# Kernel tuning notes

Measured on AMD Instinct MI355X. Metric: run time of the kernel, lower is better.

## Reference

```python
import jax, jax.numpy as jnp
import numpy as np

N, E, F_IN, H, D = 50000, 800000, 128, 4, 32
NEG_SLOPE = 0.2

def setup_inputs() -> dict:
    key = jax.random.key(0)
    ks = jax.random.split(key, 8)
    x = jax.random.normal(ks[0], (N, F_IN), dtype=jnp.float32)
    src = jax.random.randint(ks[1], (E,), 0, N, dtype=jnp.int32)
    dst = jax.random.randint(ks[2], (E,), 0, N, dtype=jnp.int32)
    s = 1.0 / np.sqrt(F_IN)
    W_src = jax.random.uniform(ks[3], (F_IN, H * D), jnp.float32, -s, s)
    b_src = jnp.zeros((H * D,), jnp.float32)
    W_dst = jax.random.uniform(ks[4], (F_IN, H * D), jnp.float32, -s, s)
    b_dst = jnp.zeros((H * D,), jnp.float32)
    attn = jax.random.normal(ks[5], (H, D), dtype=jnp.float32) / np.sqrt(D)
    return {"x": x, "src": src, "dst": dst, "W_src": W_src, "b_src": b_src,
            "W_dst": W_dst, "b_dst": b_dst, "attn": attn}

def reference(x, src, dst, W_src, b_src, W_dst, b_dst, attn):
    n = x.shape[0]
    # dense projections: [N, H, D]
    fs = (x @ W_src + b_src).reshape(n, H, D)
    fd = (x @ W_dst + b_dst).reshape(n, H, D)
    # GATv2 edge score: a^T leaky_relu(W_l x_u + W_r x_v)
    e = jax.nn.leaky_relu(fs[src] + fd[dst], NEG_SLOPE)  # [E, H, D]
    score = jnp.einsum('ehd,hd->eh', e, attn)            # [E, H]
    # segment softmax over incoming edges of each dst node
    smax = jax.ops.segment_max(score, dst, num_segments=n)
    smax = jnp.where(jnp.isfinite(smax), smax, 0.0)
    ex = jnp.exp(score - smax[dst])
    denom = jax.ops.segment_sum(ex, dst, num_segments=n)
    alpha = ex / denom[dst]                              # [E, H]
    # scatter-weighted aggregation of src features
    h = jax.ops.segment_sum(alpha[:, :, None] * fs[src], dst, num_segments=n)
    h = jax.nn.relu(h)                                   # activation=relu
    return h.reshape(n, H * D)
```

## Files before the change

kernel.cpp:

```cpp
#include <hip/hip_runtime.h>
#include <hip/hip_fp16.h>

#define NN 50000
#define NE 800000
#define FIN 128
#define NH 4
#define HD 32
#define FOUT 128
#define NEG 0.2f
#define NB_W    ((256 * FIN + 255) / 256)
#define N_GEMM  391
#define NBKT    98
#define CHUNK   4096
#define NCHUNK  ((NE + CHUNK - 1) / CHUNK)
#define GB_GRID (NCHUNK * 3)
#define BCAP    12288

typedef __attribute__((ext_vector_type(8))) short bf16x8;
typedef __attribute__((ext_vector_type(4))) float f32x4;

__device__ __forceinline__ uint f2bf_u(float f) {
    uint u = __float_as_uint(f);
    u += 0x7FFF + ((u >> 16) & 1);
    return u >> 16;
}
__device__ __forceinline__ ushort f2bf(float f) { return (ushort)f2bf_u(f); }

template<int CTRL>
__device__ __forceinline__ float dpp_add(float x) {
    int y = __builtin_amdgcn_update_dpp(0, __float_as_int(x), CTRL, 0xF, 0xF, false);
    return x + __int_as_float(y);
}
#define DPP_QUAD_XOR1 0xB1
#define DPP_QUAD_XOR2 0x4E

__device__ __forceinline__ __half2 u2h(uint u) { return __builtin_bit_cast(__half2, u); }
__device__ __forceinline__ uint h2u(__half2 h) { return __builtin_bit_cast(uint, h); }

__device__ __forceinline__ __half2 hmax2(__half2 a, __half2 b) {
    uint r, ua = h2u(a), ub = h2u(b);
    asm("v_pk_max_f16 %0, %1, %2" : "=v"(r) : "v"(ua), "v"(ub));
    return u2h(r);
}

__global__ __launch_bounds__(256) void hist_wt_k(
    const int* __restrict__ dst, int* __restrict__ chunk_hist,
    const float* __restrict__ Wsrc, const float* __restrict__ Wdst,
    ushort* __restrict__ Wt)
{
    __shared__ int hist[NBKT];
    const int b = blockIdx.x;
    const int tid = threadIdx.x;
    if (b < NCHUNK) {
        const int e0 = b * CHUNK;
        for (int t = tid; t < NBKT; t += 256) hist[t] = 0;
        __syncthreads();
        #pragma unroll
        for (int k = 0; k < 16; ++k) {
            const int e = e0 + k * 256 + tid;
            if (e < NE) atomicAdd(&hist[dst[e] >> 9], 1);
        }
        __syncthreads();
        for (int t = tid; t < NBKT; t += 256)
            chunk_hist[b * NBKT + t] = hist[t];
    } else {
        int t = (b - NCHUNK) * 256 + tid;
        if (t >= 256 * FIN) return;
        int n = t >> 7, k = t & 127;
        float v = (n < 128) ? Wsrc[k * 128 + n] : Wdst[k * 128 + (n - 128)];
        Wt[t] = f2bf(v);
    }
}

__global__ __launch_bounds__(256) void scan_chunks_k(
    const int* __restrict__ chunk_hist, int* __restrict__ chunk_base, int* __restrict__ btotal)
{
    __shared__ int sh[256];
    const int b = blockIdx.x, t = threadIdx.x;
    const int v = (t < NCHUNK) ? chunk_hist[t * NBKT + b] : 0;
    sh[t] = v;
    __syncthreads();
    for (int off = 1; off < 256; off <<= 1) {
        int add = (t >= off) ? sh[t - off] : 0;
        __syncthreads();
        sh[t] += add;
        __syncthreads();
    }
    if (t < NCHUNK) chunk_base[t * NBKT + b] = sh[t] - v;
    if (t == 255) btotal[b] = sh[255];
}

__global__ __launch_bounds__(256) void scan_buckets_k(
    const int* __restrict__ btotal, int* __restrict__ bkbase,
    const float* __restrict__ attn, __half* __restrict__ attn_h)
{
    __shared__ int sh[256];
    const int t = threadIdx.x;
    const int v = (t < NBKT) ? btotal[t] : 0;
    sh[t] = v;
    __syncthreads();
    for (int off = 1; off < 256; off <<= 1) {
        int add = (t >= off) ? sh[t - off] : 0;
        __syncthreads();
        sh[t] += add;
        __syncthreads();
    }
    if (t < NBKT) bkbase[t] = sh[t] - v;
    if (t == 0) bkbase[NBKT] = NE;
    if (t < FOUT) attn_h[t] = __float2half(attn[t]);
}

__global__ __launch_bounds__(256) void gemm_scatter_k(
    const float* __restrict__ x, const ushort* __restrict__ Wt,
    const float* __restrict__ bsrc, const float* __restrict__ bdst,
    __half* __restrict__ fsfd,
    const int* __restrict__ dst, const int* __restrict__ src,
    const int* __restrict__ bkbase, const int* __restrict__ chunk_base,
    uint* __restrict__ ebuf)
{
    __shared__ ushort As[128 * 128];
    __shared__ ushort Bs[64 * 128];
    __shared__ int cur[NBKT];
    const int b = blockIdx.x;
    const int tid = threadIdx.x;

    if (b % 3 == 0) {
        const int chunk = b / 3;
        for (int t = tid; t < NBKT; t += 256)
            cur[t] = bkbase[t] + chunk_base[chunk * NBKT + t];
        __syncthreads();
        const int e0 = chunk * CHUNK;
        #pragma unroll
        for (int k = 0; k < 16; ++k) {
            const int e = e0 + k * 256 + tid;
            if (e < NE) {
                const int d = dst[e];
                const int p = atomicAdd(&cur[d >> 9], 1);
                ebuf[p] = ((uint)d << 16) | (uint)src[e];
            }
        }
        return;
    }

    const int g = b - b / 3 - 1;
    if (g >= N_GEMM) return;
    const int bm = g * 128;

    for (int q = tid; q < 128 * 16; q += 256) {
        int r = q >> 4, c16 = q & 15;
        int row = bm + r;
        uint4 o = make_uint4(0u, 0u, 0u, 0u);
        if (row < NN) {
            const float4 a = *(const float4*)&x[(size_t)row * FIN + c16 * 8];
            const float4 c = *(const float4*)&x[(size_t)row * FIN + c16 * 8 + 4];
            o.x = f2bf_u(a.x) | (f2bf_u(a.y) << 16);
            o.y = f2bf_u(a.z) | (f2bf_u(a.w) << 16);
            o.z = f2bf_u(c.x) | (f2bf_u(c.y) << 16);
            o.w = f2bf_u(c.z) | (f2bf_u(c.w) << 16);
        }
        int off = r * 256 + ((c16 * 16) ^ ((r & 7) << 4));
        *(uint4*)((char*)As + off) = o;
    }

    const int wid = tid >> 6, lane = tid & 63;
    const int wr = (wid >> 1) * 64, wc = (wid & 1) * 32;
    const int lrow = lane & 15;
    const int lk = (lane >> 4) * 16;

    #pragma unroll
    for (int ct = 0; ct < 4; ++ct) {
        if (ct > 0) __syncthreads();
        for (int q = tid; q < 64 * 16; q += 256) {
            int r = q >> 4, c16 = q & 15;
            uint4 v = *(const uint4*)&Wt[(ct * 64 + r) * FIN + c16 * 8];
            int off = r * 256 + ((c16 * 16) ^ ((r & 7) << 4));
            *(uint4*)((char*)Bs + off) = v;
        }
        __syncthreads();

        f32x4 acc[4][2] = {};
        #pragma unroll
        for (int kk = 0; kk < 4; ++kk) {
            bf16x8 a[4], bb[2];
            #pragma unroll
            for (int m = 0; m < 4; ++m) {
                int r = wr + m * 16 + lrow;
                int off = r * 256 + ((kk * 64 + lk) ^ ((r & 7) << 4));
                a[m] = *(bf16x8*)((char*)As + off);
            }
            #pragma unroll
            for (int n = 0; n < 2; ++n) {
                int r = wc + n * 16 + lrow;
                int off = r * 256 + ((kk * 64 + lk) ^ ((r & 7) << 4));
                bb[n] = *(bf16x8*)((char*)Bs + off);
            }
            #pragma unroll
            for (int m = 0; m < 4; ++m)
                #pragma unroll
                for (int n = 0; n < 2; ++n)
                    acc[m][n] = __builtin_amdgcn_mfma_f32_16x16x32_bf16(a[m], bb[n], acc[m][n], 0, 0, 0);
        }

        #pragma unroll
        for (int m = 0; m < 4; ++m) {
            #pragma unroll
            for (int n = 0; n < 2; ++n) {
                int gcol = ct * 64 + wc + n * 16 + (lane & 15);
                float bias = (gcol < 128) ? bsrc[gcol] : bdst[gcol - 128];
                #pragma unroll
                for (int r = 0; r < 4; ++r) {
                    int grow = bm + wr + m * 16 + (lane >> 4) * 4 + r;
                    if (grow < NN)
                        fsfd[(size_t)grow * 256 + gcol] = __float2half(acc[m][n][r] + bias);
                }
            }
        }
    }
}

__global__ __launch_bounds__(256) void binB_k(
    const uint* __restrict__ ebuf, const int* __restrict__ bkbase,
    int* __restrict__ rowptr, ushort* __restrict__ nbr)
{
    __shared__ int cnt_s[512];
    __shared__ int ps[256];
    __shared__ ushort buf[BCAP];
    const int b = blockIdx.x;
    const int tid = threadIdx.x;
    const int node0 = b << 9;
    const int nodes = (node0 + 512 < NN) ? 512 : (NN - node0);
    const int segbase = bkbase[b];
    const int segend  = bkbase[b + 1];
    const int seglen  = segend - segbase;

    cnt_s[tid] = 0;
    cnt_s[tid + 256] = 0;
    __syncthreads();
    for (int i = segbase + tid; i < segend; i += 256)
        atomicAdd(&cnt_s[(int)(ebuf[i] >> 16) - node0], 1);
    __syncthreads();

    const int c0 = cnt_s[2 * tid], c1 = cnt_s[2 * tid + 1];
    const int pair = c0 + c1;
    ps[tid] = pair;
    __syncthreads();
    for (int off = 1; off < 256; off <<= 1) {
        int add = (tid >= off) ? ps[tid - off] : 0;
        __syncthreads();
        ps[tid] += add;
        __syncthreads();
    }
    const int ex = ps[tid] - pair;
    __syncthreads();
    cnt_s[2 * tid] = ex;
    cnt_s[2 * tid + 1] = ex + c0;
    if (2 * tid < nodes)     rowptr[node0 + 2 * tid]     = segbase + ex;
    if (2 * tid + 1 < nodes) rowptr[node0 + 2 * tid + 1] = segbase + ex + c0;
    if (b == NBKT - 1 && tid == 0) rowptr[NN] = segend;
    __syncthreads();

    if (seglen <= BCAP) {
        for (int i = segbase + tid; i < segend; i += 256) {
            const uint e = ebuf[i];
            const int d = (int)(e >> 16) - node0;
            const int p = atomicAdd(&cnt_s[d], 1);
            buf[p] = (ushort)(e & 0xffffu);
        }
        __syncthreads();
        for (int i = tid; i < seglen; i += 256)
            nbr[segbase + i] = buf[i];
    } else {
        for (int i = segbase + tid; i < segend; i += 256) {
            const uint e = ebuf[i];
            const int d = (int)(e >> 16) - node0;
            const int p = atomicAdd(&cnt_s[d], 1);
            nbr[segbase + p] = (ushort)(e & 0xffffu);
        }
    }
}

__global__ __launch_bounds__(256) void gat_node_k(
    const __half* __restrict__ fsfd, const __half* __restrict__ attn_h,
    const int* __restrict__ rowptr, const ushort* __restrict__ nbr,
    float* __restrict__ out)
{
    const int node = blockIdx.x * 4 + (threadIdx.x >> 6);
    const int lane = threadIdx.x & 63;
    const int ql = lane & 15;
    const int q  = lane >> 4;

    const uint4 ufd = *(const uint4*)&fsfd[(size_t)node * 256 + 128 + 8 * ql];
    const __half2 fd0 = u2h(ufd.x), fd1 = u2h(ufd.y), fd2 = u2h(ufd.z), fd3 = u2h(ufd.w);
    const uint4 uav = *(const uint4*)&attn_h[8 * ql];
    const __half2 av0 = u2h(uav.x), av1 = u2h(uav.y), av2 = u2h(uav.z), av3 = u2h(uav.w);
    const __half2 k02 = __float2half2_rn(NEG);

    const int beg = rowptr[node];
    const int end = rowptr[node + 1];

    float den = 0.f;
    __half2 acc0 = u2h(0), acc1 = u2h(0), acc2 = u2h(0), acc3 = u2h(0);

    for (int i = beg; i < end; i += 16) {
        #pragma unroll
        for (int j = 0; j < 4; ++j) {
            const int idx = i + 4 * j + q;
            const bool valid = idx < end;
            const int s = nbr[valid ? idx : end - 1];
            const uint4 u = *(const uint4*)&fsfd[(size_t)s * 256 + 8 * ql];
            const __half2 f0 = u2h(u.x), f1 = u2h(u.y), f2 = u2h(u.z), f3 = u2h(u.w);
            __half2 v0 = __hadd2(f0, fd0), v1 = __hadd2(f1, fd1);
            __half2 v2 = __hadd2(f2, fd2), v3 = __hadd2(f3, fd3);
            v0 = hmax2(v0, __hmul2(v0, k02));
            v1 = hmax2(v1, __hmul2(v1, k02));
            v2 = hmax2(v2, __hmul2(v2, k02));
            v3 = hmax2(v3, __hmul2(v3, k02));
            __half2 sch = __hmul2(v0, av0);
            sch = __hfma2(v1, av1, sch);
            sch = __hfma2(v2, av2, sch);
            sch = __hfma2(v3, av3, sch);
            float sc = __low2float(sch) + __high2float(sch);
            sc = dpp_add<DPP_QUAD_XOR1>(sc);
            sc = dpp_add<DPP_QUAD_XOR2>(sc);
            float ex = __expf(sc);
            ex = valid ? ex : 0.f;
            den += ex;
            const __half2 exh = __float2half2_rn(ex);
            acc0 = __hfma2(exh, f0, acc0);
            acc1 = __hfma2(exh, f1, acc1);
            acc2 = __hfma2(exh, f2, acc2);
            acc3 = __hfma2(exh, f3, acc3);
        }
    }

    den += __shfl_xor(den, 16, 64);
    den += __shfl_xor(den, 32, 64);
    uint ua0 = h2u(acc0), ua1 = h2u(acc1), ua2 = h2u(acc2), ua3 = h2u(acc3);
    ua0 = h2u(__hadd2(u2h(ua0), u2h((uint)__shfl_xor((int)ua0, 16, 64))));
    ua1 = h2u(__hadd2(u2h(ua1), u2h((uint)__shfl_xor((int)ua1, 16, 64))));
    ua2 = h2u(__hadd2(u2h(ua2), u2h((uint)__shfl_xor((int)ua2, 16, 64))));
    ua3 = h2u(__hadd2(u2h(ua3), u2h((uint)__shfl_xor((int)ua3, 16, 64))));
    ua0 = h2u(__hadd2(u2h(ua0), u2h((uint)__shfl_xor((int)ua0, 32, 64))));
    ua1 = h2u(__hadd2(u2h(ua1), u2h((uint)__shfl_xor((int)ua1, 32, 64))));
    ua2 = h2u(__hadd2(u2h(ua2), u2h((uint)__shfl_xor((int)ua2, 32, 64))));
    ua3 = h2u(__hadd2(u2h(ua3), u2h((uint)__shfl_xor((int)ua3, 32, 64))));

    if (q == 0) {
        const float inv = (den > 0.f) ? 1.f / den : 0.f;
        float4 o0, o1;
        o0.x = fmaxf(__low2float(u2h(ua0))  * inv, 0.f);
        o0.y = fmaxf(__high2float(u2h(ua0)) * inv, 0.f);
        o0.z = fmaxf(__low2float(u2h(ua1))  * inv, 0.f);
        o0.w = fmaxf(__high2float(u2h(ua1)) * inv, 0.f);
        o1.x = fmaxf(__low2float(u2h(ua2))  * inv, 0.f);
        o1.y = fmaxf(__high2float(u2h(ua2)) * inv, 0.f);
        o1.z = fmaxf(__low2float(u2h(ua3))  * inv, 0.f);
        o1.w = fmaxf(__high2float(u2h(ua3)) * inv, 0.f);
        *(float4*)&out[(size_t)node * FOUT + 8 * ql] = o0;
        *(float4*)&out[(size_t)node * FOUT + 8 * ql + 4] = o1;
    }
}

extern "C" void kernel_launch(void* const* d_in, const int* in_sizes, int n_in,
                              void* d_out, int out_size, void* d_ws, size_t ws_size,
                              hipStream_t stream)
{
    const float* x    = (const float*)d_in[0];
    const int*   src  = (const int*)d_in[1];
    const int*   dst  = (const int*)d_in[2];
    const float* Wsrc = (const float*)d_in[3];
    const float* bsrc = (const float*)d_in[4];
    const float* Wdst = (const float*)d_in[5];
    const float* bdst = (const float*)d_in[6];
    const float* attn = (const float*)d_in[7];
    float* out = (float*)d_out;

    ushort* Wt      = (ushort*)d_ws;
    __half* fsfd    = (__half*)(Wt + 256 * FIN);
    int* chunk_hist = (int*)(fsfd + (size_t)NN * 256);
    int* chunk_base = chunk_hist + NCHUNK * NBKT;
    int* btotal     = chunk_base + NCHUNK * NBKT;
    int* bkbase     = btotal + NBKT;
    int* rowptr     = bkbase + NBKT + 1;
    uint* ebuf      = (uint*)(rowptr + NN + 1);
    ushort* nbr     = (ushort*)(ebuf + NE);
    __half* attn_h  = (__half*)(nbr + NE);

    hist_wt_k<<<NCHUNK + NB_W, 256, 0, stream>>>(dst, chunk_hist, Wsrc, Wdst, Wt);
    scan_chunks_k<<<NBKT, 256, 0, stream>>>(chunk_hist, chunk_base, btotal);
    scan_buckets_k<<<1, 256, 0, stream>>>(btotal, bkbase, attn, attn_h);
    gemm_scatter_k<<<GB_GRID, 256, 0, stream>>>(x, Wt, bsrc, bdst, fsfd,
                                                dst, src, bkbase, chunk_base, ebuf);
    binB_k<<<NBKT, 256, 0, stream>>>(ebuf, bkbase, rowptr, nbr);
    gat_node_k<<<(NN + 3) / 4, 256, 0, stream>>>(fsfd, attn_h, rowptr, nbr, out);
}
```

Baseline: 91.39 us.

## Fold bucket scans into scatter blocks to drop two kernel launches

Removes the two separate scan kernels. Each scatter block in the fused gemm/scatter kernel now recomputes the per-bucket totals and its own chunk prefix straight from the chunk histogram, and chunk 0 writes the global bucket bases. The attention half-precision conversion moves into the histogram kernel. This saves two launches and their dependency gaps, at the cost of every scatter block reading the whole histogram (196x98 ints) and running a redundant block scan.

After: 89.45 us. 2.1% less time.

```diff
diff --git a/kernel.cpp b/kernel.cpp
--- a/kernel.cpp
+++ b/kernel.cpp
@@ -46,7 +46,8 @@
 __global__ __launch_bounds__(256) void hist_wt_k(
     const int* __restrict__ dst, int* __restrict__ chunk_hist,
     const float* __restrict__ Wsrc, const float* __restrict__ Wdst,
-    ushort* __restrict__ Wt)
+    ushort* __restrict__ Wt,
+    const float* __restrict__ attn, __half* __restrict__ attn_h)
 {
     __shared__ int hist[NBKT];
     const int b = blockIdx.x;
@@ -64,6 +65,7 @@
         for (int t = tid; t < NBKT; t += 256)
             chunk_hist[b * NBKT + t] = hist[t];
     } else {
+        if (b == NCHUNK && tid < FOUT) attn_h[tid] = __float2half(attn[tid]);
         int t = (b - NCHUNK) * 256 + tid;
         if (t >= 256 * FIN) return;
         int n = t >> 7, k = t & 127;
@@ -72,62 +74,44 @@
     }
 }
 
-__global__ __launch_bounds__(256) void scan_chunks_k(
-    const int* __restrict__ chunk_hist, int* __restrict__ chunk_base, int* __restrict__ btotal)
-{
-    __shared__ int sh[256];
-    const int b = blockIdx.x, t = threadIdx.x;
-    const int v = (t < NCHUNK) ? chunk_hist[t * NBKT + b] : 0;
-    sh[t] = v;
-    __syncthreads();
-    for (int off = 1; off < 256; off <<= 1) {
-        int add = (t >= off) ? sh[t - off] : 0;
-        __syncthreads();
-        sh[t] += add;
-        __syncthreads();
-    }
-    if (t < NCHUNK) chunk_base[t * NBKT + b] = sh[t] - v;
-    if (t == 255) btotal[b] = sh[255];
-}
-
-__global__ __launch_bounds__(256) void scan_buckets_k(
-    const int* __restrict__ btotal, int* __restrict__ bkbase,
-    const float* __restrict__ attn, __half* __restrict__ attn_h)
-{
-    __shared__ int sh[256];
-    const int t = threadIdx.x;
-    const int v = (t < NBKT) ? btotal[t] : 0;
-    sh[t] = v;
-    __syncthreads();
-    for (int off = 1; off < 256; off <<= 1) {
-        int add = (t >= off) ? sh[t - off] : 0;
-        __syncthreads();
-        sh[t] += add;
-        __syncthreads();
-    }
-    if (t < NBKT) bkbase[t] = sh[t] - v;
-    if (t == 0) bkbase[NBKT] = NE;
-    if (t < FOUT) attn_h[t] = __float2half(attn[t]);
-}
-
 __global__ __launch_bounds__(256) void gemm_scatter_k(
     const float* __restrict__ x, const ushort* __restrict__ Wt,
     const float* __restrict__ bsrc, const float* __restrict__ bdst,
     __half* __restrict__ fsfd,
     const int* __restrict__ dst, const int* __restrict__ src,
-    const int* __restrict__ bkbase, const int* __restrict__ chunk_base,
+    const int* __restrict__ chunk_hist, int* __restrict__ bkbase,
     uint* __restrict__ ebuf)
 {
     __shared__ ushort As[128 * 128];
     __shared__ ushort Bs[64 * 128];
     __shared__ int cur[NBKT];
+    __shared__ int ps[256];
     const int b = blockIdx.x;
     const int tid = threadIdx.x;
 
     if (b % 3 == 0) {
         const int chunk = b / 3;
-        for (int t = tid; t < NBKT; t += 256)
-            cur[t] = bkbase[t] + chunk_base[chunk * NBKT + t];
+        int total = 0, part = 0;
+        if (tid < NBKT) {
+            for (int c = 0; c < NCHUNK; ++c) {
+                const int h = chunk_hist[c * NBKT + tid];
+                total += h;
+                part += (c < chunk) ? h : 0;
+            }
+        }
+        ps[tid] = (tid < NBKT) ? total : 0;
+        __syncthreads();
+        for (int off = 1; off < 256; off <<= 1) {
+            int add = (tid >= off) ? ps[tid - off] : 0;
+            __syncthreads();
+            ps[tid] += add;
+            __syncthreads();
+        }
+        if (tid < NBKT) cur[tid] = (ps[tid] - total) + part;
+        if (chunk == 0) {
+            if (tid < NBKT) bkbase[tid] = ps[tid] - total;
+            if (tid == 0) bkbase[NBKT] = NE;
+        }
         __syncthreads();
         const int e0 = chunk * CHUNK;
         #pragma unroll
@@ -378,19 +362,15 @@
     ushort* Wt      = (ushort*)d_ws;
     __half* fsfd    = (__half*)(Wt + 256 * FIN);
     int* chunk_hist = (int*)(fsfd + (size_t)NN * 256);
-    int* chunk_base = chunk_hist + NCHUNK * NBKT;
-    int* btotal     = chunk_base + NCHUNK * NBKT;
-    int* bkbase     = btotal + NBKT;
+    int* bkbase     = chunk_hist + NCHUNK * NBKT;
     int* rowptr     = bkbase + NBKT + 1;
     uint* ebuf      = (uint*)(rowptr + NN + 1);
     ushort* nbr     = (ushort*)(ebuf + NE);
     __half* attn_h  = (__half*)(nbr + NE);
 
-    hist_wt_k<<<NCHUNK + NB_W, 256, 0, stream>>>(dst, chunk_hist, Wsrc, Wdst, Wt);
-    scan_chunks_k<<<NBKT, 256, 0, stream>>>(chunk_hist, chunk_base, btotal);
-    scan_buckets_k<<<1, 256, 0, stream>>>(btotal, bkbase, attn, attn_h);
+    hist_wt_k<<<NCHUNK + NB_W, 256, 0, stream>>>(dst, chunk_hist, Wsrc, Wdst, Wt, attn, attn_h);
     gemm_scatter_k<<<GB_GRID, 256, 0, stream>>>(x, Wt, bsrc, bdst, fsfd,
-                                                dst, src, bkbase, chunk_base, ebuf);
+                                                dst, src, chunk_hist, bkbase, ebuf);
     binB_k<<<NBKT, 256, 0, stream>>>(ebuf, bkbase, rowptr, nbr);
     gat_node_k<<<(NN + 3) / 4, 256, 0, stream>>>(fsfd, attn_h, rowptr, nbr, out);
 }
```
